# Kernel optimization log

Measured on AMD Instinct MI355X. Metric: run time of the kernel, lower is better.

## Reference

```python
import jax, jax.numpy as jnp
import numpy as np

N = 50000      # nodes
E = 800000     # edges (before self loops)
IN = 128       # in_channels
H = 4          # heads
C = 32         # hidden_channels (per head)
D = H * C      # concat output dim = 128
NEG_SLOPE = 0.2
LN_EPS = 1e-5


def setup_inputs() -> dict:
    key = jax.random.key(0)
    ks = jax.random.split(key, 24)
    def p(k, shape, s=0.1):
        return jax.random.normal(k, shape, dtype=jnp.float32) * s
    inp = {
        "x": p(ks[0], (N, IN), 1.0),
        "edge_index": jax.random.randint(ks[1], (2, E), 0, N, dtype=jnp.int32),
    }
    i = 2
    for l, ind in [(0, IN), (1, D)]:
        inp[f"Wl{l}"] = p(ks[i], (ind, D)); i += 1
        inp[f"bl{l}"] = p(ks[i], (D,), 0.02); i += 1
        inp[f"Wr{l}"] = p(ks[i], (ind, D)); i += 1
        inp[f"br{l}"] = p(ks[i], (D,), 0.02); i += 1
        inp[f"att{l}"] = p(ks[i], (H, C)); i += 1
        inp[f"Wres{l}"] = p(ks[i], (ind, D)); i += 1
        inp[f"bias{l}"] = p(ks[i], (D,), 0.02); i += 1
        inp[f"g{l}"] = jnp.ones((D,), jnp.float32)
        inp[f"be{l}"] = jnp.zeros((D,), jnp.float32)
    return inp


def _gatv2_layer(x, src, dst, Wl, bl, Wr, br, att, Wres, bias):
    """GATv2Conv with concat heads, add_self_loops already applied, residual."""
    n = x.shape[0]
    xl = (x @ Wl + bl).reshape(n, H, C)   # source transform
    xr = (x @ Wr + br).reshape(n, H, C)   # target transform
    # edge-level attention logits: e = a . LeakyReLU(xl[j] + xr[i])  [E, H]
    eh = jax.nn.leaky_relu(xl[src] + xr[dst], negative_slope=NEG_SLOPE)  # [E,H,C]
    score = jnp.einsum('ehc,hc->eh', eh, att)                            # [E,H]
    # segment softmax over incoming edges of each destination node
    smax = jax.ops.segment_max(score, dst, num_segments=n)               # [N,H]
    ex = jnp.exp(score - smax[dst])
    ssum = jax.ops.segment_sum(ex, dst, num_segments=n)                  # [N,H]
    alpha = ex / ssum[dst]                                               # [E,H]
    msg = xl[src] * alpha[:, :, None]                                    # [E,H,C]
    out = jax.ops.segment_sum(msg, dst, num_segments=n).reshape(n, D)
    return out + x @ Wres + bias  # residual (bias=False linear) + final bias


def _layernorm_relu(x, g, b):
    mu = jnp.mean(x, axis=-1, keepdims=True)
    var = jnp.mean(jnp.square(x - mu), axis=-1, keepdims=True)
    return jax.nn.relu((x - mu) * jax.lax.rsqrt(var + LN_EPS) * g + b)


def reference(x, edge_index,
              Wl0, bl0, Wr0, br0, att0, Wres0, bias0, g0, be0,
              Wl1, bl1, Wr1, br1, att1, Wres1, bias1, g1, be1):
    n = x.shape[0]
    loops = jnp.arange(n, dtype=edge_index.dtype)
    src = jnp.concatenate([edge_index[0], loops])  # add_self_loops=True
    dst = jnp.concatenate([edge_index[1], loops])
    h = _gatv2_layer(x, src, dst, Wl0, bl0, Wr0, br0, att0, Wres0, bias0)
    h = _layernorm_relu(h, g0, be0)
    h = _gatv2_layer(h, src, dst, Wl1, bl1, Wr1, br1, att1, Wres1, bias1)
    h = _layernorm_relu(h, g1, be1)
    return h
```

## Files before the change

### kernel.cpp

```cpp
#include <hip/hip_runtime.h>
#include <math.h>

#define D 128
#define LRELU 0.2f
#define LN_EPS 1e-5f
#define INV_LN2 1.4426950408889634f

typedef __attribute__((ext_vector_type(8))) short short8;
typedef __attribute__((ext_vector_type(8))) unsigned short ushort8;
typedef __attribute__((ext_vector_type(4))) float f32x4;
typedef __attribute__((ext_vector_type(2))) float f32x2;
typedef __attribute__((ext_vector_type(2))) unsigned int u32x2;

static __device__ __forceinline__ unsigned short f2bf(float f) {
    union { float f; unsigned u; } a; a.f = f;
    unsigned r = a.u + 0x7FFFu + ((a.u >> 16) & 1u);
    return (unsigned short)(r >> 16);
}

static __device__ __forceinline__ f32x2 pk_add(f32x2 a, f32x2 b) {
    f32x2 d; asm("v_pk_add_f32 %0, %1, %2" : "=v"(d) : "v"(a), "v"(b)); return d;
}
static __device__ __forceinline__ f32x2 pk_mul(f32x2 a, f32x2 b) {
    f32x2 d; asm("v_pk_mul_f32 %0, %1, %2" : "=v"(d) : "v"(a), "v"(b)); return d;
}
static __device__ __forceinline__ f32x2 pk_fma(f32x2 a, f32x2 b, f32x2 c) {
    f32x2 d; asm("v_pk_fma_f32 %0, %1, %2, %3" : "=v"(d) : "v"(a), "v"(b), "v"(c)); return d;
}
static __device__ __forceinline__ f32x2 pk_abs(f32x2 a) {
    u32x2 u = __builtin_bit_cast(u32x2, a);
    u &= 0x7FFFFFFFu;
    return __builtin_bit_cast(f32x2, u);
}
static __device__ __forceinline__ f32x2 bf2x(unsigned u) {
    f32x2 r;
    r.x = __uint_as_float(u << 16);
    r.y = __uint_as_float(u & 0xFFFF0000u);
    return r;
}

static __device__ __forceinline__ float red4_dpp(float p) {
    int v = __builtin_amdgcn_update_dpp(0, __builtin_bit_cast(int, p), 0xB1, 0xf, 0xf, true);
    p += __builtin_bit_cast(float, v);
    v = __builtin_amdgcn_update_dpp(0, __builtin_bit_cast(int, p), 0x4E, 0xf, 0xf, true);
    p += __builtin_bit_cast(float, v);
    return p;
}

#define SCB 256


__global__ __launch_bounds__(256) void k_prep(
    const int* __restrict__ dst, int* __restrict__ deg, int* __restrict__ rank, int E, int N,
    const float* __restrict__ X, ushort* __restrict__ Xb, int Mp,
    const float* __restrict__ W0, const float* __restrict__ W1, const float* __restrict__ W2,
    const float* __restrict__ W3, const float* __restrict__ W4, const float* __restrict__ W5,
    ushort* __restrict__ Wp, int nCR, int nCV)
{
    const int bx = blockIdx.x;
    const int tid = threadIdx.x;
    if (bx < nCR) {
        int e = bx * 256 + tid;
        if (e < E + N) {
            int d = (e < E) ? dst[e] : e - E;
            rank[e] = atomicAdd(&deg[d], 1);
        }
    } else if (bx < nCR + nCV) {
        int idx = (bx - nCR) * 256 + tid;
        if (idx >= Mp * (D / 4)) return;
        ushort4 o;
        if (idx < N * (D / 4)) {
            float4 v = ((const float4*)X)[idx];
            o.x = f2bf(v.x); o.y = f2bf(v.y); o.z = f2bf(v.z); o.w = f2bf(v.w);
        } else {
            o = make_ushort4(0, 0, 0, 0);
        }
        ((ushort4*)Xb)[idx] = o;
    } else {
        int bid = bx - nCR - nCV;
        int m = bid >> 6;
        int o = ((bid & 63) << 8) + tid;
        const float* W;
        if (m == 0) W = W0; else if (m == 1) W = W1; else if (m == 2) W = W2;
        else if (m == 3) W = W3; else if (m == 4) W = W4; else W = W5;
        int j  = o & 7;
        int l  = (o >> 3) & 63;
        int ct = (o >> 9) & 7;
        int kc = o >> 12;
        int k   = kc * 32 + ((l >> 4) << 3) + j;
        int col = (ct << 4) + (l & 15);
        Wp[m * 16384 + o] = f2bf(W[k * D + col]);
    }
}


__global__ __launch_bounds__(SCB) void partial_kernel(const int* __restrict__ deg,
                                                      int* __restrict__ bsum, int n) {
    int i = blockIdx.x * SCB + threadIdx.x;
    int v = (i < n) ? deg[i] : 0;
    #pragma unroll
    for (int o = 32; o >= 1; o >>= 1) v += __shfl_xor(v, o);
    __shared__ int ws[4];
    if ((threadIdx.x & 63) == 0) ws[threadIdx.x >> 6] = v;
    __syncthreads();
    if (threadIdx.x == 0) bsum[blockIdx.x] = ws[0] + ws[1] + ws[2] + ws[3];
}

__global__ __launch_bounds__(SCB) void scan_bsum_kernel(int* __restrict__ bsum, int nb) {
    int t = threadIdx.x;
    int v = (t < nb) ? bsum[t] : 0;
    int incl = v;
    #pragma unroll
    for (int o = 1; o < 64; o <<= 1) {
        int u = __shfl_up(incl, o);
        if ((t & 63) >= o) incl += u;
    }
    __shared__ int wp[4];
    if ((t & 63) == 63) wp[t >> 6] = incl;
    __syncthreads();
    int add = 0;
    for (int k = 0; k < (t >> 6); ++k) add += wp[k];
    incl += add;
    if (t < nb) bsum[t] = incl - v;
}

__global__ __launch_bounds__(SCB) void write_off_kernel(const int* __restrict__ deg,
                                                        const int* __restrict__ boff,
                                                        int* __restrict__ off, int n) {
    int t = threadIdx.x;
    int i = blockIdx.x * SCB + t;
    int v = (i < n) ? deg[i] : 0;
    int incl = v;
    #pragma unroll
    for (int o = 1; o < 64; o <<= 1) {
        int u = __shfl_up(incl, o);
        if ((t & 63) >= o) incl += u;
    }
    __shared__ int wp[4];
    if ((t & 63) == 63) wp[t >> 6] = incl;
    __syncthreads();
    int add = boff[blockIdx.x];
    for (int k = 0; k < (t >> 6); ++k) add += wp[k];
    int excl = add + incl - v;
    if (i < n) off[i] = excl;
    if (i == n - 1) off[n] = excl + v;
}


static __device__ __forceinline__ void gemm_body(
    int bxg, int seg, int tid,
    const ushort* __restrict__ Xb, const ushort* __restrict__ Wp,
    const float* __restrict__ bl, const float* __restrict__ br,
    ushort* __restrict__ XLb, ushort* __restrict__ XRb, float* __restrict__ RES)
{
    const int l = tid & 63;
    const int wave = tid >> 6;
    const int wr = wave >> 1, wc = wave & 1;
    const int brow = bxg * 128 + wr * 64;
    const ushort* W = Wp + seg * 16384;

    f32x4 acc[4][4] = {};
    const int arow = brow + (l & 15);
    const int koff = (l >> 4) * 8;

    #pragma unroll
    for (int kc = 0; kc < 4; ++kc) {
        short8 A[4], B[4];
        #pragma unroll
        for (int at = 0; at < 4; ++at)
            A[at] = *(const short8*)&Xb[(size_t)(arow + at * 16) * D + kc * 32 + koff];
        #pragma unroll
        for (int ct = 0; ct < 4; ++ct) {
            int ctg = wc * 4 + ct;
            B[ct] = *(const short8*)&W[(((kc * 8 + ctg) * 64) + l) * 8];
        }
        #pragma unroll
        for (int at = 0; at < 4; ++at)
            #pragma unroll
            for (int ct = 0; ct < 4; ++ct)
                acc[at][ct] = __builtin_amdgcn_mfma_f32_16x16x32_bf16(A[at], B[ct], acc[at][ct], 0, 0, 0);
    }

    const int c = l & 15;
    const int r0 = (l >> 4) * 4;
    const float* bias = (seg == 0) ? bl : ((seg == 1) ? br : nullptr);
    #pragma unroll
    for (int ct = 0; ct < 4; ++ct) {
        int gcol = wc * 64 + ct * 16 + c;
        float bv = bias ? bias[gcol] : 0.f;
        #pragma unroll
        for (int at = 0; at < 4; ++at) {
            #pragma unroll
            for (int r = 0; r < 4; ++r) {
                int grow = brow + at * 16 + r0 + r;
                float v = acc[at][ct][r] + bv;
                size_t off = (size_t)grow * D + gcol;
                if (seg == 0)      XLb[off] = f2bf(v);
                else if (seg == 1) XRb[off] = f2bf(v);
                else               RES[off] = v;
            }
        }
    }
}

__global__ __launch_bounds__(256) void k_mid(
    const int* __restrict__ src, const int* __restrict__ dst,
    const int* __restrict__ off, const int* __restrict__ rank,
    int* __restrict__ csrc, int E, int N, int nSC, int nblk,
    const ushort* __restrict__ Xb, const ushort* __restrict__ Wp,
    const float* __restrict__ bl, const float* __restrict__ br,
    ushort* __restrict__ XLb, ushort* __restrict__ XRb, float* __restrict__ RES)
{
    const int bx = blockIdx.x;
    if (bx < nSC) {
        int e = bx * 256 + threadIdx.x;
        if (e < E + N) {
            int d  = (e < E) ? dst[e] : e - E;
            int sc = (e < E) ? src[e] : e - E;
            int p = off[d] + rank[e];
            __builtin_nontemporal_store(sc, &csrc[p]);
        }
    } else {
        int bid = bx - nSC;
        int seg = bid / nblk;
        int bxg = bid - seg * nblk;
        gemm_body(bxg, seg, threadIdx.x, Xb, Wp, bl, br, XLb, XRb, RES);
    }
}

__global__ __launch_bounds__(256) void gemm_mfma(
    const ushort* __restrict__ Xb, const ushort* __restrict__ Wp,
    const float* __restrict__ bl, const float* __restrict__ br,
    ushort* __restrict__ XLb, ushort* __restrict__ XRb, float* __restrict__ RES)
{
    gemm_body(blockIdx.x, blockIdx.y, threadIdx.x, Xb, Wp, bl, br, XLb, XRb, RES);
}


__global__ __launch_bounds__(256) void gat_node(
    const ushort* __restrict__ XLb, const ushort* __restrict__ XRb, const float* __restrict__ RES,
    const float* __restrict__ att, const float* __restrict__ bias,
    const float* __restrict__ g, const float* __restrict__ be,
    const int* __restrict__ off, const int* __restrict__ csrc,
    float* __restrict__ OUTf, ushort* __restrict__ OUTb)
{
    const int l = threadIdx.x & 63;
    const int i = blockIdx.x * 16 + (threadIdx.x >> 6) * 4 + (l >> 4);
    const int f = (l & 15) * 8;
    const unsigned ibase = ((unsigned)i << 7) + f;
    const int lb = l & 48;

    f32x2 at06[4], at04[4];
    #pragma unroll
    for (int k = 0; k < 4; ++k) {
        float2 a = *(const float2*)&att[f + k * 2];
        f32x2 av; av.x = a.x; av.y = a.y;
        at06[k] = av * (0.6f * INV_LN2);
        at04[k] = av * (0.4f * INV_LN2);
    }

    uint4 xru = *(const uint4*)&XRb[ibase];
    f32x2 xr2[4];
    xr2[0] = bf2x(xru.x); xr2[1] = bf2x(xru.y); xr2[2] = bf2x(xru.z); xr2[3] = bf2x(xru.w);

    const int e0 = off[i], e1 = off[i + 1];
    const int len = e1 - e0;
    int mx = max(len, __shfl_xor(len, 16));
    mx = max(mx, __shfl_xor(mx, 32));

    float m = -1e30f, s = 0.f;
    f32x2 a2[4] = {};

    for (int c0 = 0; c0 < mx; c0 += 16) {
        int myj = csrc[min(e0 + c0 + (l & 15), e1 - 1)];
        const int rem = mx - c0;
        const int kleft = len - c0;

        #pragma unroll
        for (int bb = 0; bb < 4; ++bb) {
            if (bb * 4 >= rem) break;
            int s0 = __shfl(myj, lb + bb * 4 + 0);
            int s1 = __shfl(myj, lb + bb * 4 + 1);
            int s2 = __shfl(myj, lb + bb * 4 + 2);
            int s3 = __shfl(myj, lb + bb * 4 + 3);
            uint4 u[4];
            u[0] = *(const uint4*)&XLb[((unsigned)s0 << 7) + f];
            u[1] = *(const uint4*)&XLb[((unsigned)s1 << 7) + f];
            u[2] = *(const uint4*)&XLb[((unsigned)s2 << 7) + f];
            u[3] = *(const uint4*)&XLb[((unsigned)s3 << 7) + f];

            const int kb = kleft - bb * 4;
            f32x2 xp[4][4];
            float p[4];
            #pragma unroll
            for (int j = 0; j < 4; ++j) {
                xp[j][0] = bf2x(u[j].x);
                xp[j][1] = bf2x(u[j].y);
                xp[j][2] = bf2x(u[j].z);
                xp[j][3] = bf2x(u[j].w);
                f32x2 v0 = pk_add(xp[j][0], xr2[0]);
                f32x2 pj2 = pk_mul(v0, at06[0]);
                pj2 = pk_fma(pk_abs(v0), at04[0], pj2);
                #pragma unroll
                for (int k = 1; k < 4; ++k) {
                    f32x2 v = pk_add(xp[j][k], xr2[k]);
                    pj2 = pk_fma(v, at06[k], pj2);
                    pj2 = pk_fma(pk_abs(v), at04[k], pj2);
                }
                float pj = pj2.x + pj2.y;
                pj = red4_dpp(pj);
                p[j] = (j < kb) ? pj : -1e30f;
            }
            float pmax = fmaxf(fmaxf(p[0], p[1]), fmaxf(p[2], p[3]));
            float nm = fmaxf(m, pmax);
            float so = exp2f(m - nm);
            float w0 = exp2f(p[0] - nm), w1 = exp2f(p[1] - nm);
            float w2 = exp2f(p[2] - nm), w3 = exp2f(p[3] - nm);
            s = s * so + ((w0 + w1) + (w2 + w3));
            f32x2 so2; so2.x = so; so2.y = so;
            f32x2 w02; w02.x = w0; w02.y = w0;
            f32x2 w12; w12.x = w1; w12.y = w1;
            f32x2 w22; w22.x = w2; w22.y = w2;
            f32x2 w32; w32.x = w3; w32.y = w3;
            #pragma unroll
            for (int k = 0; k < 4; ++k) {
                f32x2 t = pk_mul(xp[0][k], w02);
                t = pk_fma(xp[1][k], w12, t);
                t = pk_fma(xp[2][k], w22, t);
                t = pk_fma(xp[3][k], w32, t);
                a2[k] = pk_fma(a2[k], so2, t);
            }
            m = nm;
        }
    }

    const float4 rsA = *(const float4*)&RES[ibase];
    const float4 rsB = *(const float4*)&RES[ibase + 4];
    const float4 biA = *(const float4*)&bias[f];
    const float4 biB = *(const float4*)&bias[f + 4];
    float inv = 1.f / s;
    float r0 = a2[0].x * inv + rsA.x + biA.x;
    float r1 = a2[0].y * inv + rsA.y + biA.y;
    float r2 = a2[1].x * inv + rsA.z + biA.z;
    float r3 = a2[1].y * inv + rsA.w + biA.w;
    float r4 = a2[2].x * inv + rsB.x + biB.x;
    float r5 = a2[2].y * inv + rsB.y + biB.y;
    float r6 = a2[3].x * inv + rsB.z + biB.z;
    float r7 = a2[3].y * inv + rsB.w + biB.w;

    float sum = ((r0 + r1) + (r2 + r3)) + ((r4 + r5) + (r6 + r7));
    float sq  = ((r0 * r0 + r1 * r1) + (r2 * r2 + r3 * r3))
              + ((r4 * r4 + r5 * r5) + (r6 * r6 + r7 * r7));
    #pragma unroll
    for (int o = 8; o >= 1; o >>= 1) {
        sum += __shfl_xor(sum, o);
        sq  += __shfl_xor(sq, o);
    }
    float mu  = sum * (1.f / 128.f);
    float var = sq * (1.f / 128.f) - mu * mu;
    float isd = rsqrtf(var + LN_EPS);
    const float4 gvA = *(const float4*)&g[f];
    const float4 gvB = *(const float4*)&g[f + 4];
    const float4 bvA = *(const float4*)&be[f];
    const float4 bvB = *(const float4*)&be[f + 4];
    float o0 = fmaxf((r0 - mu) * isd * gvA.x + bvA.x, 0.f);
    float o1 = fmaxf((r1 - mu) * isd * gvA.y + bvA.y, 0.f);
    float o2 = fmaxf((r2 - mu) * isd * gvA.z + bvA.z, 0.f);
    float o3 = fmaxf((r3 - mu) * isd * gvA.w + bvA.w, 0.f);
    float o4 = fmaxf((r4 - mu) * isd * gvB.x + bvB.x, 0.f);
    float o5 = fmaxf((r5 - mu) * isd * gvB.y + bvB.y, 0.f);
    float o6 = fmaxf((r6 - mu) * isd * gvB.z + bvB.z, 0.f);
    float o7 = fmaxf((r7 - mu) * isd * gvB.w + bvB.w, 0.f);

    if (OUTb) {
        ushort8 ob;
        ob[0] = f2bf(o0); ob[1] = f2bf(o1); ob[2] = f2bf(o2); ob[3] = f2bf(o3);
        ob[4] = f2bf(o4); ob[5] = f2bf(o5); ob[6] = f2bf(o6); ob[7] = f2bf(o7);
        *(ushort8*)&OUTb[ibase] = ob;
    } else {
        *(float4*)&OUTf[ibase]     = make_float4(o0, o1, o2, o3);
        *(float4*)&OUTf[ibase + 4] = make_float4(o4, o5, o6, o7);
    }
}


extern "C" void kernel_launch(void* const* d_in, const int* in_sizes, int n_in,
                              void* d_out, int out_size, void* d_ws, size_t ws_size,
                              hipStream_t stream)
{
    const float* x    = (const float*)d_in[0];
    const int*   ei   = (const int*)d_in[1];
    const float* Wl0  = (const float*)d_in[2];
    const float* bl0  = (const float*)d_in[3];
    const float* Wr0  = (const float*)d_in[4];
    const float* br0  = (const float*)d_in[5];
    const float* att0 = (const float*)d_in[6];
    const float* Wres0= (const float*)d_in[7];
    const float* bias0= (const float*)d_in[8];
    const float* g0   = (const float*)d_in[9];
    const float* be0  = (const float*)d_in[10];
    const float* Wl1  = (const float*)d_in[11];
    const float* bl1  = (const float*)d_in[12];
    const float* Wr1  = (const float*)d_in[13];
    const float* br1  = (const float*)d_in[14];
    const float* att1 = (const float*)d_in[15];
    const float* Wres1= (const float*)d_in[16];
    const float* bias1= (const float*)d_in[17];
    const float* g1   = (const float*)d_in[18];
    const float* be1  = (const float*)d_in[19];

    const int N  = in_sizes[0] / D;
    const int E  = in_sizes[1] / 2;
    const int E2 = E + N;
    const int nblk = (N + 127) / 128;
    const int Mp = nblk * 128;
    const int nb = (N + SCB - 1) / SCB;

    char* w = (char*)d_ws;
    ushort* Xb  = (ushort*)w; w += (size_t)Mp * D * 2;
    ushort* Hb  = (ushort*)w; w += (size_t)Mp * D * 2;
    ushort* XLb = (ushort*)w; w += (size_t)Mp * D * 2;
    ushort* XRb = (ushort*)w; w += (size_t)Mp * D * 2;
    float*  RES = (float*)w;  w += (size_t)Mp * D * 4;
    ushort* Wp  = (ushort*)w; w += (size_t)6 * 16384 * 2;
    int* deg     = (int*)w; w += (size_t)N * 4;
    int* off     = (int*)w; w += (size_t)(N + 1) * 4;
    int* rank    = (int*)w; w += (size_t)E2 * 4;
    int* bsum    = (int*)w; w += (size_t)nb * 4;
    int* csrc    = (int*)w; w += (size_t)E2 * 4;

    const int* srcp = ei;
    const int* dstp = ei + E;

    const int nCR = (E2 + 255) / 256;
    const int nCV = (Mp * (D / 4) + 255) / 256;
    const int nPW = 6 * 64;
    const int nSC = nCR;
    const int nGM = nblk * 3;

    hipMemsetAsync(deg, 0, (size_t)N * 4, stream);
    k_prep<<<nCR + nCV + nPW, 256, 0, stream>>>(dstp, deg, rank, E, N,
                                                x, Xb, Mp,
                                                Wl0, Wr0, Wres0, Wl1, Wr1, Wres1,
                                                Wp, nCR, nCV);
    partial_kernel<<<nb, SCB, 0, stream>>>(deg, bsum, N);
    scan_bsum_kernel<<<1, SCB, 0, stream>>>(bsum, nb);
    write_off_kernel<<<nb, SCB, 0, stream>>>(deg, bsum, off, N);

    k_mid<<<nSC + nGM, 256, 0, stream>>>(srcp, dstp, off, rank, csrc, E, N, nSC, nblk,
                                         Xb, Wp, bl0, br0, XLb, XRb, RES);

    const int gatg = N / 16;
    dim3 ggrid(nblk, 3);

    gat_node<<<gatg, 256, 0, stream>>>(XLb, XRb, RES, att0, bias0, g0, be0, off, csrc, nullptr, Hb);
    gemm_mfma<<<ggrid, 256, 0, stream>>>(Hb, Wp + 3 * 16384, bl1, br1, XLb, XRb, RES);
    gat_node<<<gatg, 256, 0, stream>>>(XLb, XRb, RES, att1, bias1, g1, be1, off, csrc, (float*)d_out, nullptr);
}
```

Before: 212.4 us.

## Build CSR via bucketed two-pass partition with shared-memory atomics

Per-edge global atomics on the degree array are replaced by a bucketed partition. Each block histograms a chunk of edges into 128-node buckets in shared memory and reserves space per bucket with one global atomic. It then scatters packed (src, local dst) words into per-bucket buffers. A new per-bucket kernel computes degrees with shared-memory atomics, and the CSR scatter now works one bucket at a time with shared-memory cursors. This is meant to cut contended global atomics and make the csrc writes more local. The trade-offs are an extra kernel launch and a fixed per-bucket capacity (4096) plus a cap of 512 buckets; exceeding either would silently corrupt results.

```diff
diff --git a/kernel.cpp b/kernel.cpp
--- a/kernel.cpp
+++ b/kernel.cpp
@@ -5,6 +5,10 @@
 #define LRELU 0.2f
 #define LN_EPS 1e-5f
 #define INV_LN2 1.4426950408889634f
+
+#define NBMAX 512
+#define CAP 4096
+#define P1CHUNK 8192
 
 typedef __attribute__((ext_vector_type(8))) short short8;
 typedef __attribute__((ext_vector_type(8))) unsigned short ushort8;
@@ -51,22 +55,41 @@
 
 
 __global__ __launch_bounds__(256) void k_prep(
-    const int* __restrict__ dst, int* __restrict__ deg, int* __restrict__ rank, int E, int N,
+    const int* __restrict__ srcp, const int* __restrict__ dstp,
+    int* __restrict__ bcur, unsigned* __restrict__ ebuf, int E, int N,
     const float* __restrict__ X, ushort* __restrict__ Xb, int Mp,
     const float* __restrict__ W0, const float* __restrict__ W1, const float* __restrict__ W2,
     const float* __restrict__ W3, const float* __restrict__ W4, const float* __restrict__ W5,
-    ushort* __restrict__ Wp, int nCR, int nCV)
+    ushort* __restrict__ Wp, int nP1, int nCV)
 {
     const int bx = blockIdx.x;
     const int tid = threadIdx.x;
-    if (bx < nCR) {
-        int e = bx * 256 + tid;
-        if (e < E + N) {
-            int d = (e < E) ? dst[e] : e - E;
-            rank[e] = atomicAdd(&deg[d], 1);
-        }
-    } else if (bx < nCR + nCV) {
-        int idx = (bx - nCR) * 256 + tid;
+    if (bx < nP1) {
+        __shared__ int h[NBMAX];
+        const int E2 = E + N;
+        const int e0 = bx * P1CHUNK;
+        const int e1 = min(e0 + P1CHUNK, E2);
+        for (int t = tid; t < NBMAX; t += 256) h[t] = 0;
+        __syncthreads();
+        for (int e = e0 + tid; e < e1; e += 256) {
+            int d = (e < E) ? dstp[e] : e - E;
+            atomicAdd(&h[d >> 7], 1);
+        }
+        __syncthreads();
+        for (int b = tid; b < NBMAX; b += 256) {
+            int c = h[b];
+            h[b] = c ? atomicAdd(&bcur[b], c) : 0;
+        }
+        __syncthreads();
+        for (int e = e0 + tid; e < e1; e += 256) {
+            int d  = (e < E) ? dstp[e] : e - E;
+            int sc = (e < E) ? srcp[e] : e - E;
+            int b = d >> 7;
+            int pos = atomicAdd(&h[b], 1) & (CAP - 1);
+            ebuf[(size_t)b * CAP + pos] = ((unsigned)sc << 7) | (unsigned)(d & 127);
+        }
+    } else if (bx < nP1 + nCV) {
+        int idx = (bx - nP1) * 256 + tid;
         if (idx >= Mp * (D / 4)) return;
         ushort4 o;
         if (idx < N * (D / 4)) {
@@ -77,7 +100,7 @@
         }
         ((ushort4*)Xb)[idx] = o;
     } else {
-        int bid = bx - nCR - nCV;
+        int bid = bx - nP1 - nCV;
         int m = bid >> 6;
         int o = ((bid & 63) << 8) + tid;
         const float* W;
@@ -91,6 +114,24 @@
         int col = (ct << 4) + (l & 15);
         Wp[m * 16384 + o] = f2bf(W[k * D + col]);
     }
+}
+
+
+__global__ __launch_bounds__(256) void bhist_kernel(const unsigned* __restrict__ ebuf,
+                                                    const int* __restrict__ bcur,
+                                                    int* __restrict__ deg, int N) {
+    const int b = blockIdx.x;
+    const int base = b << 7;
+    __shared__ int h[128];
+    if (threadIdx.x < 128) h[threadIdx.x] = 0;
+    __syncthreads();
+    const int cnt = min(bcur[b], CAP);
+    for (int k = threadIdx.x; k < cnt; k += 256) {
+        unsigned v = ebuf[(size_t)b * CAP + k];
+        atomicAdd(&h[v & 127], 1);
+    }
+    __syncthreads();
+    if (threadIdx.x < 128 && base + threadIdx.x < N) deg[base + threadIdx.x] = h[threadIdx.x];
 }
 
 
@@ -203,25 +244,30 @@
     }
 }
 
+
 __global__ __launch_bounds__(256) void k_mid(
-    const int* __restrict__ src, const int* __restrict__ dst,
-    const int* __restrict__ off, const int* __restrict__ rank,
-    int* __restrict__ csrc, int E, int N, int nSC, int nblk,
+    const unsigned* __restrict__ ebuf, const int* __restrict__ bcur,
+    const int* __restrict__ off, int* __restrict__ csrc, int N, int NB, int nblk,
     const ushort* __restrict__ Xb, const ushort* __restrict__ Wp,
     const float* __restrict__ bl, const float* __restrict__ br,
     ushort* __restrict__ XLb, ushort* __restrict__ XRb, float* __restrict__ RES)
 {
     const int bx = blockIdx.x;
-    if (bx < nSC) {
-        int e = bx * 256 + threadIdx.x;
-        if (e < E + N) {
-            int d  = (e < E) ? dst[e] : e - E;
-            int sc = (e < E) ? src[e] : e - E;
-            int p = off[d] + rank[e];
-            __builtin_nontemporal_store(sc, &csrc[p]);
+    if (bx < NB) {
+        const int b = bx;
+        const int base = b << 7;
+        __shared__ int cur[128];
+        if (threadIdx.x < 128)
+            cur[threadIdx.x] = (base + threadIdx.x < N) ? off[base + threadIdx.x] : 0;
+        __syncthreads();
+        const int cnt = min(bcur[b], CAP);
+        for (int k = threadIdx.x; k < cnt; k += 256) {
+            unsigned v = ebuf[(size_t)b * CAP + k];
+            int p = atomicAdd(&cur[v & 127], 1);
+            csrc[p] = v >> 7;
         }
     } else {
-        int bid = bx - nSC;
+        int bid = bx - NB;
         int seg = bid / nblk;
         int bxg = bid - seg * nblk;
         gemm_body(bxg, seg, threadIdx.x, Xb, Wp, bl, br, XLb, XRb, RES);
@@ -415,6 +461,7 @@
     const int nblk = (N + 127) / 128;
     const int Mp = nblk * 128;
     const int nb = (N + SCB - 1) / SCB;
+    const int NB = nblk;
 
     char* w = (char*)d_ws;
     ushort* Xb  = (ushort*)w; w += (size_t)Mp * D * 2;
@@ -425,30 +472,31 @@
     ushort* Wp  = (ushort*)w; w += (size_t)6 * 16384 * 2;
     int* deg     = (int*)w; w += (size_t)N * 4;
     int* off     = (int*)w; w += (size_t)(N + 1) * 4;
-    int* rank    = (int*)w; w += (size_t)E2 * 4;
+    int* bcur    = (int*)w; w += (size_t)NBMAX * 4;
     int* bsum    = (int*)w; w += (size_t)nb * 4;
+    unsigned* ebuf = (unsigned*)w; w += (size_t)NB * CAP * 4;
     int* csrc    = (int*)w; w += (size_t)E2 * 4;
 
     const int* srcp = ei;
     const int* dstp = ei + E;
 
-    const int nCR = (E2 + 255) / 256;
+    const int nP1 = (E2 + P1CHUNK - 1) / P1CHUNK;
     const int nCV = (Mp * (D / 4) + 255) / 256;
     const int nPW = 6 * 64;
-    const int nSC = nCR;
     const int nGM = nblk * 3;
 
-    hipMemsetAsync(deg, 0, (size_t)N * 4, stream);
-    k_prep<<<nCR + nCV + nPW, 256, 0, stream>>>(dstp, deg, rank, E, N,
+    hipMemsetAsync(bcur, 0, (size_t)NBMAX * 4, stream);
+    k_prep<<<nP1 + nCV + nPW, 256, 0, stream>>>(srcp, dstp, bcur, ebuf, E, N,
                                                 x, Xb, Mp,
                                                 Wl0, Wr0, Wres0, Wl1, Wr1, Wres1,
-                                                Wp, nCR, nCV);
+                                                Wp, nP1, nCV);
+    bhist_kernel<<<NB, 256, 0, stream>>>(ebuf, bcur, deg, N);
     partial_kernel<<<nb, SCB, 0, stream>>>(deg, bsum, N);
     scan_bsum_kernel<<<1, SCB, 0, stream>>>(bsum, nb);
     write_off_kernel<<<nb, SCB, 0, stream>>>(deg, bsum, off, N);
 
-    k_mid<<<nSC + nGM, 256, 0, stream>>>(srcp, dstp, off, rank, csrc, E, N, nSC, nblk,
-                                         Xb, Wp, bl0, br0, XLb, XRb, RES);
+    k_mid<<<NB + nGM, 256, 0, stream>>>(ebuf, bcur, off, csrc, N, NB, nblk,
+                                        Xb, Wp, bl0, br0, XLb, XRb, RES);
 
     const int gatg = N / 16;
     dim3 ggrid(nblk, 3);
```

After: 191.1 us. 1.11x faster.
